# Performance work log

Hardware: AMD Instinct MI355X
Metric: run time of the kernel (lower is better)

## Reference

```python
import jax, jax.numpy as jnp
import numpy as np

B, S, D, H = 2, 2048, 1024, 16
DH = D // H  # per-head dim = 64


def setup_inputs() -> dict:
    key = jax.random.key(0)
    k0, k1, k2, k3, k4, k5 = jax.random.split(key, 6)
    x = jax.random.normal(k0, (B, S, D), dtype=jnp.float32)
    # mask: True where token is valid, False where padded ([B, S, 1] bool)
    mask = jax.random.randint(k1, (B, S, 1), 0, 2).astype(bool)
    scale = 0.02
    # Per-head projection weights stacked over heads: [H, D, DH]
    Wq = jax.random.normal(k2, (H, D, DH), dtype=jnp.float32) * scale
    Wk = jax.random.normal(k3, (H, D, DH), dtype=jnp.float32) * scale
    Wv = jax.random.normal(k4, (H, D, DH), dtype=jnp.float32) * scale
    # Output projection, torch Linear convention [out, in]: y = out @ Wo.T
    Wo = jax.random.normal(k5, (D, D), dtype=jnp.float32) * scale
    return {"x": x, "mask": mask, "Wq": Wq, "Wk": Wk, "Wv": Wv, "Wo": Wo}


def reference(x, mask, Wq, Wk, Wv, Wo):
    # Batched per-head projections (equivalent to the per-head Linear loop)
    q = jnp.einsum('bsd,hde->bhse', x, Wq)  # [B,H,S,DH]
    k = jnp.einsum('bsd,hde->bhse', x, Wk)
    v = jnp.einsum('bsd,hde->bhse', x, Wv)
    scale = 1.0 / np.sqrt(DH).astype(np.float32)
    scores = jnp.einsum('bhqe,bhke->bhqk', q, k) * scale  # [B,H,S,S]
    key_mask = mask[:, None, None, :, 0]   # [B,1,1,S]
    qry_mask = mask[:, None, :, :]          # [B,1,S,1]
    # masked keys get -1e10 added (same as original: +(~key_mask)*-1e10)
    scores = scores + (~key_mask) * jnp.float32(-1e10)
    attn = jax.nn.softmax(scores, axis=-1)
    attn = attn * qry_mask                  # zero rows for padded queries
    ctx = jnp.einsum('bhqk,bhke->bhqe', attn, v)  # [B,H,S,DH]
    # concat heads along last dim (head h -> contiguous slice, matches torch.cat)
    out = ctx.transpose(0, 2, 1, 3).reshape(B, S, D)
    return out @ Wo.T
```

## Files before the change

### kernel.cpp

```cpp
#include <hip/hip_runtime.h>
#include <hip/hip_bf16.h>

typedef __attribute__((ext_vector_type(8))) short sh8;
typedef __attribute__((ext_vector_type(4))) float f32x4;

#define LDC 136
#define QSCALE 0.18033688f
#define KMBF16 0xF14Au

#define EXP2F(x) __builtin_amdgcn_exp2f(x)

__device__ __forceinline__ void glds16(const unsigned short* g, unsigned short* l){
  __builtin_amdgcn_global_load_lds(
      (const __attribute__((address_space(1))) unsigned int*)g,
      (__attribute__((address_space(3))) unsigned int*)l, 16, 0, 0);
}

__device__ __forceinline__ unsigned short f2bf(float f){
  union { float f; unsigned u; } c; c.f = f;
  unsigned u = c.u;
  u += 0x7fffu + ((u >> 16) & 1u);
  return (unsigned short)(u >> 16);
}

__device__ __forceinline__ unsigned long long pack4bf(float a, float b, float c, float d){
  __hip_bfloat162 lo = __float22bfloat162_rn(make_float2(a, b));
  __hip_bfloat162 hi = __float22bfloat162_rn(make_float2(c, d));
  union { unsigned u[2]; unsigned long long ull; } pk;
  pk.u[0] = *(unsigned*)&lo; pk.u[1] = *(unsigned*)&hi;
  return pk.ull;
}

__global__ __launch_bounds__(256) void cvt_bf16_2(const float* __restrict__ s0,
                                                  unsigned short* __restrict__ d0, int n0,
                                                  const float* __restrict__ s1,
                                                  unsigned short* __restrict__ d1, int n1){
  int i = blockIdx.x*256 + threadIdx.x;
  const float* s; unsigned short* d;
  if (i < n0){ s = s0; d = d0; }
  else if (i < n0 + n1){ s = s1; d = d1; i -= n0; }
  else return;
  float4 v = ((const float4*)s)[i];
  ushort4 o;
  o.x = f2bf(v.x); o.y = f2bf(v.y); o.z = f2bf(v.z); o.w = f2bf(v.w);
  ((ushort4*)d)[i] = o;
}

__global__ __launch_bounds__(256) void transpose_w(const float* __restrict__ Wq,
                                                   const float* __restrict__ Wk,
                                                   const float* __restrict__ Wv,
                                                   unsigned short* __restrict__ wt){
  __shared__ float tile[64][65];
  int idx = blockIdx.x;
  int jm = idx >> 8;
  int rest = idx & 255;
  int h = rest >> 4, dt = rest & 15;
  const float* src = (jm==0 ? Wq : (jm==1 ? Wk : Wv)) + (size_t)h*65536;
  int t = threadIdx.x;
  {
    int r = t >> 2, c0 = (t & 3)*16;
    for (int i=0;i<4;++i){
      float4 v = *(const float4*)&src[(size_t)(dt*64 + r)*64 + c0 + i*4];
      tile[r][c0+i*4+0]=v.x; tile[r][c0+i*4+1]=v.y; tile[r][c0+i*4+2]=v.z; tile[r][c0+i*4+3]=v.w;
    }
  }
  __syncthreads();
  {
    int e = t >> 2, r0 = (t & 3)*16;
    int j = jm*1024 + h*64 + e;
    __align__(16) unsigned short buf[16];
    for (int i=0;i<16;++i) buf[i] = f2bf(tile[r0+i][e]);
    *(uint4*)&wt[(size_t)j*1024 + dt*64 + r0    ] = *(uint4*)&buf[0];
    *(uint4*)&wt[(size_t)j*1024 + dt*64 + r0 + 8] = *(uint4*)&buf[8];
  }
}

template<int BM>
__global__ __launch_bounds__(256) void gemm_bt(const unsigned short* __restrict__ A,
                                               const unsigned short* __restrict__ Bt,
                                               unsigned short* __restrict__ Cq,
                                               unsigned short* __restrict__ Ck,
                                               unsigned short* __restrict__ Cv,
                                               float* __restrict__ Cf,
                                               int M, int N, int K, int mode){
  constexpr int MI = BM/32;
  constexpr int SMEMN = (BM == 128) ? 17408 : (BM*64 + 8192);
  __shared__ __align__(16) unsigned short smem[SMEMN];
  unsigned short* As = smem;
  unsigned short* Bs = smem + BM*64;
  const int t = threadIdx.x;
  const int w = t >> 6, lane = t & 63, l15 = lane & 15, quad = lane >> 4;

  int lin = blockIdx.y * gridDim.x + blockIdx.x;
  int gn = gridDim.x, gm = gridDim.y;
  int per = 8 * gn;
  int gid = lin / per, rem = lin % per;
  int mfirst = gid * 8;
  int msz = (gm - mfirst) < 8 ? (gm - mfirst) : 8;
  const int m0 = (mfirst + rem % msz) * BM;
  const int n0 = (rem / msz) * 128;

  const int wm = (w >> 1)*(BM/2), wn = (w & 1)*64;
  const int lr8 = lane >> 3;
  const int gc8 = (lane & 7) ^ lr8;
  const int h7 = l15 & 7;
  f32x4 acc[MI][4] = {};

  for (int k0 = 0; k0 < K; k0 += 64){
    __syncthreads();
    for (int p = 0; p < BM/32; ++p){
      int rbase = p*32 + w*8;
      glds16(&A [(size_t)(m0 + rbase + lr8)*K + k0 + gc8*8], &As[rbase*64]);
    }
    for (int p = 0; p < 4; ++p){
      int rbase = p*32 + w*8;
      glds16(&Bt[(size_t)(n0 + rbase + lr8)*K + k0 + gc8*8], &Bs[rbase*64]);
    }
    __syncthreads();
    for (int kk = 0; kk < 2; ++kk){
      const int cs = (((kk<<2) + quad) ^ h7) * 8;
      sh8 aF[MI], bF[4];
      for (int i = 0; i < MI; ++i)
        aF[i] = *(const sh8*)&As[(wm + i*16 + l15)*64 + cs];
      for (int i = 0; i < 4; ++i)
        bF[i] = *(const sh8*)&Bs[(wn + i*16 + l15)*64 + cs];
      for (int mi = 0; mi < MI; ++mi)
        for (int ni = 0; ni < 4; ++ni)
          acc[mi][ni] = __builtin_amdgcn_mfma_f32_16x16x32_bf16(aF[mi], bF[ni], acc[mi][ni], 0, 0, 0);
    }
  }

  if (mode == 2){
    for (int mi = 0; mi < MI; ++mi){
      int rowb = m0 + wm + mi*16 + quad*4;
      for (int ni = 0; ni < 4; ++ni){
        int col = n0 + wn + ni*16 + l15;
        for (int r = 0; r < 4; ++r)
          Cf[(size_t)(rowb + r)*N + col] = acc[mi][ni][r];
      }
    }
    return;
  }

  if constexpr (BM == 128){
    __syncthreads();
    unsigned short* Ct = smem;
    const bool isv = (n0 >= 2048);
    const float cscale = (n0 < 1024) ? QSCALE : 1.0f;
    for (int mi = 0; mi < 4; ++mi){
      for (int ni = 0; ni < 4; ++ni){
        for (int r = 0; r < 4; ++r){
          int lr = wm + mi*16 + quad*4 + r;
          int lc = wn + ni*16 + l15;
          unsigned short bv = f2bf(acc[mi][ni][r] * cscale);
          if (isv) Ct[lc*LDC + lr] = bv;
          else     Ct[lr*LDC + lc] = bv;
        }
      }
    }
    __syncthreads();

    const int b = m0 >> 11, sbase = m0 & 2047;
    const int hbase = (n0 & 1023) >> 6;
    if (!isv){
      unsigned short* dst = (n0 < 1024) ? Cq : Ck;
      for (int i = 0; i < 8; ++i){
        int s  = i*16 + (t >> 4);
        int hh = (t >> 3) & 1;
        int c  = t & 7;
        uint4 val = *(const uint4*)&Ct[s*LDC + hh*64 + c*8];
        int h = hbase + hh;
        *(uint4*)&dst[((size_t)(b*16 + h)*2048 + sbase + s)*64 + c*8] = val;
      }
    } else {
      for (int i = 0; i < 8; ++i){
        int ecol = i*16 + (t >> 4);
        int s0   = (t & 15)*8;
        uint4 val = *(const uint4*)&Ct[ecol*LDC + s0];
        int hh = ecol >> 6, e = ecol & 63;
        int h = hbase + hh;
        *(uint4*)&Cv[((size_t)(b*16 + h)*64 + e)*2048 + sbase + s0] = val;
      }
    }
  }
}

__global__ __launch_bounds__(512) void flash_attn(const unsigned short* __restrict__ q,
                                                  const unsigned short* __restrict__ k,
                                                  const unsigned short* __restrict__ vt,
                                                  const int* __restrict__ mask,
                                                  unsigned short* __restrict__ ctx){
  __shared__ __align__(16) unsigned short Ks[2][4096];
  __shared__ __align__(16) unsigned short Vs[2][4096];
  __shared__ __align__(16) unsigned short Ps[8][1024];
  __shared__ __align__(16) unsigned short kmb[2048];

  const int idx = blockIdx.x;
  const int xcd = idx & 7, sub = idx >> 3;
  const int bh = xcd*4 + (sub & 3);
  const int qt = sub >> 2;
  const int b = bh >> 4, h = bh & 15;
  const int t = threadIdx.x;
  const int w = t >> 6, lane = t & 63, l15 = lane & 15, quad = lane >> 4;
  const size_t base = (size_t)bh * 2048 * 64;

  const unsigned short* qp0 = q + base + (size_t)(qt*128 + w*16 + l15)*64;
  sh8 qf[2];
  qf[0] = *(const sh8*)(qp0 +      quad*8);
  qf[1] = *(const sh8*)(qp0 + 32 + quad*8);

  {
    int4 m0 = ((const int4*)(mask + b*2048))[t];
    __align__(8) unsigned short tmp[4];
    tmp[0] = m0.x ? 0 : KMBF16; tmp[1] = m0.y ? 0 : KMBF16;
    tmp[2] = m0.z ? 0 : KMBF16; tmp[3] = m0.w ? 0 : KMBF16;
    *(unsigned long long*)&kmb[t*4] = *(unsigned long long*)tmp;
  }

  const int lr8 = lane >> 3;
  const int gc8 = (lane & 7) ^ lr8;
  const int h7 = l15 & 7;
  const int cs0 = ((quad    ) ^ h7) * 8;
  const int cs1 = ((quad + 4) ^ h7) * 8;
  const int pw_off = (quad & 1)*4;
  const int pr0 = ((0*4 + quad) ^ h7) * 8;
  const int pr1 = ((1*4 + quad) ^ h7) * 8;

  auto stageKV = [&](int kt, int bb){
    int r0 = w*8;
    glds16(&k [base + (size_t)(kt*64 + r0 + lr8)*64 + gc8*8], &Ks[bb][r0*64]);
    glds16(&vt[base + (size_t)(r0 + lr8)*2048 + kt*64 + gc8*8], &Vs[bb][r0*64]);
  };

  float la[4] = {};
  f32x4 O[4] = {};

  stageKV(0, 0);
  for (int kt = 0; kt < 32; ++kt){
    const int bb = kt & 1;
    __syncthreads();
    if (kt + 1 < 32) stageKV(kt + 1, bb ^ 1);

    for (int mt = 0; mt < 4; ++mt){
      sh8 a0 = *(const sh8*)&Ks[bb][(mt*16 + l15)*64 + cs0];
      sh8 a1 = *(const sh8*)&Ks[bb][(mt*16 + l15)*64 + cs1];
      unsigned long long kq = *(const unsigned long long*)&kmb[kt*64 + mt*16 + quad*4];
      unsigned d0 = (unsigned)kq, d1 = (unsigned)(kq >> 32);
      f32x4 a;
      a[0] = __uint_as_float(d0 << 16);
      a[1] = __uint_as_float(d0 & 0xFFFF0000u);
      a[2] = __uint_as_float(d1 << 16);
      a[3] = __uint_as_float(d1 & 0xFFFF0000u);
      const int pwc = (((mt*2 + (quad>>1)) ^ h7) * 8) + pw_off;
      a = __builtin_amdgcn_mfma_f32_16x16x32_bf16(a0, qf[0], a, 0, 0, 0);
      a = __builtin_amdgcn_mfma_f32_16x16x32_bf16(a1, qf[1], a, 0, 0, 0);
      float e0 = EXP2F(a[0]); la[0] += e0;
      float e1 = EXP2F(a[1]); la[1] += e1;
      float e2 = EXP2F(a[2]); la[2] += e2;
      float e3 = EXP2F(a[3]); la[3] += e3;
      *(unsigned long long*)&Ps[w][l15*64 + pwc] = pack4bf(e0, e1, e2, e3);
    }

    sh8 pf0 = *(const sh8*)&Ps[w][l15*64 + pr0];
    sh8 pf1 = *(const sh8*)&Ps[w][l15*64 + pr1];
    for (int et = 0; et < 4; ++et){
      sh8 vf0 = *(const sh8*)&Vs[bb][(et*16 + l15)*64 + cs0];
      O[et] = __builtin_amdgcn_mfma_f32_16x16x32_bf16(vf0, pf0, O[et], 0, 0, 0);
    }
    for (int et = 0; et < 4; ++et){
      sh8 vf1 = *(const sh8*)&Vs[bb][(et*16 + l15)*64 + cs1];
      O[et] = __builtin_amdgcn_mfma_f32_16x16x32_bf16(vf1, pf1, O[et], 0, 0, 0);
    }
  }

  {
    float l_i = (la[0] + la[1]) + (la[2] + la[3]);
    l_i += __shfl_xor(l_i, 16);
    l_i += __shfl_xor(l_i, 32);
    int srow = qt*128 + w*16 + l15;
    bool qm = (kmb[srow] == 0);
    float inv = (qm && l_i > 0.f) ? 1.f/l_i : 0.f;
    unsigned short* crow = ctx + (((size_t)b*2048 + srow)*16 + h)*64;
    for (int et = 0; et < 4; ++et)
      *(unsigned long long*)&crow[et*16 + quad*4] =
        pack4bf(O[et][0]*inv, O[et][1]*inv, O[et][2]*inv, O[et][3]*inv);
  }
}

extern "C" void kernel_launch(void* const* d_in, const int* in_sizes, int n_in,
                              void* d_out, int out_size, void* d_ws, size_t ws_size,
                              hipStream_t stream){
  const float* x  = (const float*)d_in[0];
  const int* mask = (const int*)  d_in[1];
  const float* Wq = (const float*)d_in[2];
  const float* Wk = (const float*)d_in[3];
  const float* Wv = (const float*)d_in[4];
  const float* Wo = (const float*)d_in[5];
  float* out = (float*)d_out;

  char* ws = (char*)d_ws;
  unsigned short* x_bf  = (unsigned short*)(ws);
  unsigned short* wt    = (unsigned short*)(ws + 8388608);
  unsigned short* wo_bf = (unsigned short*)(ws + 14680064);
  unsigned short* qb    = (unsigned short*)(ws + 16777216);
  unsigned short* kb    = (unsigned short*)(ws + 25165824);
  unsigned short* vtb   = (unsigned short*)(ws + 33554432);
  unsigned short* ctx   = (unsigned short*)(ws + 41943040);

  cvt_bf16_2<<<5120, 256, 0, stream>>>(x, x_bf, 1048576, Wo, wo_bf, 262144);
  transpose_w<<<768, 256, 0, stream>>>(Wq, Wk, Wv, wt);
  gemm_bt<128><<<dim3(24, 32), 256, 0, stream>>>(x_bf, wt, qb, kb, vtb, nullptr, 4096, 3072, 1024, 0);
  flash_attn<<<512, 512, 0, stream>>>(qb, kb, vtb, mask, ctx);
  gemm_bt<64><<<dim3(8, 64), 256, 0, stream>>>(ctx, wo_bf, nullptr, nullptr, nullptr, out, 4096, 1024, 1024, 2);
}
```

Baseline: 202.0 us.

## Double-buffer GEMM shared-memory tiles and simplify block swizzle

Splits shared memory into two A/B buffers so the global-to-LDS loads for the next K tile are issued while MFMAs run on the current tile, leaving one barrier per K step instead of two. This is meant to hide global load latency behind compute in the projection GEMMs. It doubles LDS use per block, which can lower occupancy. It also simplifies the grouped block-index mapping by assuming the M-block count is a multiple of 8.

```diff
diff --git a/kernel.cpp b/kernel.cpp
--- a/kernel.cpp
+++ b/kernel.cpp
@@ -84,21 +84,20 @@
                                                float* __restrict__ Cf,
                                                int M, int N, int K, int mode){
   constexpr int MI = BM/32;
-  constexpr int SMEMN = (BM == 128) ? 17408 : (BM*64 + 8192);
+  constexpr int ABUF = BM*64;
+  constexpr int DBUFN = 2*ABUF + 2*8192;
+  constexpr int SMEMN = (DBUFN > 17408) ? DBUFN : 17408;
   __shared__ __align__(16) unsigned short smem[SMEMN];
-  unsigned short* As = smem;
-  unsigned short* Bs = smem + BM*64;
   const int t = threadIdx.x;
   const int w = t >> 6, lane = t & 63, l15 = lane & 15, quad = lane >> 4;
 
   int lin = blockIdx.y * gridDim.x + blockIdx.x;
-  int gn = gridDim.x, gm = gridDim.y;
+  int gn = gridDim.x;
   int per = 8 * gn;
   int gid = lin / per, rem = lin % per;
-  int mfirst = gid * 8;
-  int msz = (gm - mfirst) < 8 ? (gm - mfirst) : 8;
-  const int m0 = (mfirst + rem % msz) * BM;
-  const int n0 = (rem / msz) * 128;
+  int j = rem / gn, nc = rem % gn;
+  const int m0 = (gid*8 + j) * BM;
+  const int n0 = nc * 128;
 
   const int wm = (w >> 1)*(BM/2), wn = (w & 1)*64;
   const int lr8 = lane >> 3;
@@ -106,24 +105,34 @@
   const int h7 = l15 & 7;
   f32x4 acc[MI][4] = {};
 
-  for (int k0 = 0; k0 < K; k0 += 64){
-    __syncthreads();
+  auto stage = [&](int k0, int bb){
+    unsigned short* as = smem + bb*ABUF;
+    unsigned short* bs = smem + 2*ABUF + bb*8192;
     for (int p = 0; p < BM/32; ++p){
       int rbase = p*32 + w*8;
-      glds16(&A [(size_t)(m0 + rbase + lr8)*K + k0 + gc8*8], &As[rbase*64]);
+      glds16(&A [(size_t)(m0 + rbase + lr8)*K + k0 + gc8*8], &as[rbase*64]);
     }
     for (int p = 0; p < 4; ++p){
       int rbase = p*32 + w*8;
-      glds16(&Bt[(size_t)(n0 + rbase + lr8)*K + k0 + gc8*8], &Bs[rbase*64]);
-    }
+      glds16(&Bt[(size_t)(n0 + rbase + lr8)*K + k0 + gc8*8], &bs[rbase*64]);
+    }
+  };
+
+  const int NS = K >> 6;
+  stage(0, 0);
+  for (int ks = 0; ks < NS; ++ks){
+    const int bb = ks & 1;
     __syncthreads();
+    if (ks + 1 < NS) stage((ks+1)*64, bb ^ 1);
+    const unsigned short* as = smem + bb*ABUF;
+    const unsigned short* bs = smem + 2*ABUF + bb*8192;
     for (int kk = 0; kk < 2; ++kk){
       const int cs = (((kk<<2) + quad) ^ h7) * 8;
       sh8 aF[MI], bF[4];
       for (int i = 0; i < MI; ++i)
-        aF[i] = *(const sh8*)&As[(wm + i*16 + l15)*64 + cs];
+        aF[i] = *(const sh8*)&as[(wm + i*16 + l15)*64 + cs];
       for (int i = 0; i < 4; ++i)
-        bF[i] = *(const sh8*)&Bs[(wn + i*16 + l15)*64 + cs];
+        bF[i] = *(const sh8*)&bs[(wn + i*16 + l15)*64 + cs];
       for (int mi = 0; mi < MI; ++mi)
         for (int ni = 0; ni < 4; ++ni)
           acc[mi][ni] = __builtin_amdgcn_mfma_f32_16x16x32_bf16(aF[mi], bF[ni], acc[mi][ni], 0, 0, 0);
```

Result: faster. 184.4 us (-8.7%).
